# Kernel optimization log

Measured on AMD Instinct MI355X. Metric: run time of the kernel, lower is better.

## Reference

```python
import jax, jax.numpy as jnp
import numpy as np

T, H, E, I, K = 2048, 2048, 16, 512, 2
ROUTED_SCALE = 1.5   # config.moe_router_scaling_factor
SWIGLU_LIMIT = 7.0   # config.swiglu_limits[layer_id]


def setup_inputs() -> dict:
    key = jax.random.key(0)
    k1, k2, k3, k4, k5 = jax.random.split(key, 5)
    hidden_states = jax.random.normal(k1, (T, H), jnp.float32)
    gate_w = jax.random.normal(k2, (E, H), jnp.float32) * 0.02
    router_bias = jax.random.normal(k3, (E,), jnp.float32) * 0.01
    w13 = jax.random.normal(k4, (E, 2 * I, H), jnp.float32) * 0.02  # [gate; up] fused
    w2 = jax.random.normal(k5, (E, H, I), jnp.float32) * 0.02
    return {"hidden_states": hidden_states, "gate_w": gate_w,
            "router_bias": router_bias, "w13": w13, "w2": w2, "top_k": K}


def reference(hidden_states, gate_w, router_bias, w13, w2, top_k):
    n_tok = hidden_states.shape[0]
    n_exp = gate_w.shape[0]
    # fp32 gate (need_fp32_gate=True)
    router_logits = hidden_states.astype(jnp.float32) @ gate_w.T          # [T, E]
    scores = jax.nn.sigmoid(router_logits)
    # correction bias only affects expert choice, not the combine weights
    _, topk_ids = jax.lax.top_k(scores + router_bias[None, :], top_k)     # [T, K]
    topk_w = jnp.take_along_axis(scores, topk_ids, axis=1)                # [T, K]
    topk_w = topk_w / jnp.sum(topk_w, axis=1, keepdims=True)              # renormalize
    topk_w = topk_w * ROUTED_SCALE
    # scatter routing weights into dense per-expert combine weights [T, E]
    comb = jnp.zeros((n_tok, n_exp), jnp.float32)
    comb = comb.at[jnp.arange(n_tok)[:, None], topk_ids].add(topk_w)
    # expert SwiGLU MLPs, dense over experts (zero combine weight == not routed)
    gu = jnp.einsum('th,eoh->teo', hidden_states, w13)                    # [T, E, 2I]
    g, u = jnp.split(gu, 2, axis=-1)
    g = jnp.minimum(g, SWIGLU_LIMIT)                                      # gemm1_clamp_limit
    u = jnp.clip(u, -SWIGLU_LIMIT, SWIGLU_LIMIT)
    act = g * jax.nn.sigmoid(g) * u                                       # silu(gate) * up
    expert_out = jnp.einsum('tei,ehi->teh', act, w2)                      # [T, E, H]
    return jnp.einsum('teh,te->th', expert_out, comb)                     # [T, H]
```

## Files before the change

kernel.cpp:

```cpp
#include <hip/hip_runtime.h>
#include <hip/hip_bf16.h>
#include <math.h>

#define T_TOK 2048
#define H_DIM 2048
#define E_EXP 16
#define I_DIM 512
#define TWO_I 1024
#define ROUTED_SCALE 1.5f
#define SWIGLU_LIMIT 7.0f

#define BM 128
#define KC 32
#define MAX_TILES 48
#define SLOTS 6144

typedef __attribute__((ext_vector_type(8))) short bf16x8;
typedef __attribute__((ext_vector_type(4))) float f32x4;
typedef unsigned short u16;

__device__ inline u16 f2bf(float f) {
    return __builtin_bit_cast(u16, __float2bfloat16(f));
}
__device__ inline ushort4 pack4(float4 a) {
    ushort4 v;
    v.x = f2bf(a.x); v.y = f2bf(a.y); v.z = f2bf(a.z); v.w = f2bf(a.w);
    return v;
}
__device__ inline bf16x8 cvt8(float4 a, float4 b) {
    bf16x8 v;
    v[0] = (short)f2bf(a.x); v[1] = (short)f2bf(a.y);
    v[2] = (short)f2bf(a.z); v[3] = (short)f2bf(a.w);
    v[4] = (short)f2bf(b.x); v[5] = (short)f2bf(b.y);
    v[6] = (short)f2bf(b.z); v[7] = (short)f2bf(b.w);
    return v;
}

__device__ inline void gload16(const u16* g, u16* l) {
    __builtin_amdgcn_global_load_lds(
        (const __attribute__((address_space(1))) void*)(g),
        (__attribute__((address_space(3))) void*)(l), 16, 0, 0);
}
#define SCHED0() __builtin_amdgcn_sched_barrier(0)

__global__ __launch_bounds__(256) void router_kernel(
    const float* __restrict__ hs, const float* __restrict__ gw,
    const float* __restrict__ bias, int* cnt, int* tok_list, float* w_list,
    u16* __restrict__ hs_bf)
{
    int wave = threadIdx.x >> 6;
    int lane = threadIdx.x & 63;
    int t = blockIdx.x * 4 + wave;
    if (t >= T_TOK) return;
    const float* x = hs + (size_t)t * H_DIM;

    float acc[E_EXP];
#pragma unroll
    for (int e = 0; e < E_EXP; ++e) acc[e] = 0.f;

#pragma unroll 2
    for (int c = 0; c < 8; ++c) {
        int col = c * 256 + lane * 4;
        float4 xv = *(const float4*)(x + col);
        *(ushort4*)(hs_bf + (size_t)t * H_DIM + col) = pack4(xv);
#pragma unroll
        for (int e = 0; e < E_EXP; ++e) {
            float4 gv = *(const float4*)(gw + (size_t)e * H_DIM + col);
            acc[e] = fmaf(xv.x, gv.x, acc[e]);
            acc[e] = fmaf(xv.y, gv.y, acc[e]);
            acc[e] = fmaf(xv.z, gv.z, acc[e]);
            acc[e] = fmaf(xv.w, gv.w, acc[e]);
        }
    }
#pragma unroll
    for (int e = 0; e < E_EXP; ++e) {
        for (int m = 32; m >= 1; m >>= 1)
            acc[e] += __shfl_xor(acc[e], m, 64);
    }
    if (lane == 0) {
        float sc[E_EXP], bsc[E_EXP];
#pragma unroll
        for (int e = 0; e < E_EXP; ++e) {
            sc[e] = 1.f / (1.f + expf(-acc[e]));
            bsc[e] = sc[e] + bias[e];
        }
        int e0 = 0; float b0 = bsc[0];
#pragma unroll
        for (int e = 1; e < E_EXP; ++e) if (bsc[e] > b0) { b0 = bsc[e]; e0 = e; }
        int e1 = -1; float b1 = -1e30f;
#pragma unroll
        for (int e = 0; e < E_EXP; ++e) {
            if (e == e0) continue;
            if (bsc[e] > b1) { b1 = bsc[e]; e1 = e; }
        }
        float s0 = sc[e0], s1 = sc[e1];
        float inv = ROUTED_SCALE / (s0 + s1);
        int p0 = atomicAdd(&cnt[e0], 1);
        tok_list[e0 * T_TOK + p0] = t;
        w_list[e0 * T_TOK + p0] = s0 * inv;
        int p1 = atomicAdd(&cnt[e1], 1);
        tok_list[e1 * T_TOK + p1] = t;
        w_list[e1 * T_TOK + p1] = s1 * inv;
    }
}

__global__ void scatter_build(const int* __restrict__ cnt,
    const int* __restrict__ tok_list, const float* __restrict__ w_list,
    int* A_tok, float* A_w, int* tile_e, int* tile_r0)
{
    int c[E_EXP], offs[E_EXP + 1];
    offs[0] = 0;
#pragma unroll
    for (int e = 0; e < E_EXP; ++e) {
        c[e] = cnt[e];
        offs[e + 1] = offs[e] + ((c[e] + BM - 1) & ~(BM - 1));
    }
    int idx = blockIdx.x * 256 + threadIdx.x;
    int e = idx >> 11;
    int pos = idx & (T_TOK - 1);
    int ce = c[e];
    int pe = (ce + BM - 1) & ~(BM - 1);
    if (pos < ce) {
        A_tok[offs[e] + pos] = tok_list[idx];
        A_w[offs[e] + pos] = w_list[idx];
    } else if (pos < pe) {
        A_tok[offs[e] + pos] = -1;
        A_w[offs[e] + pos] = 0.f;
    }
    if (idx == 0) {
        int nt = 0;
        for (int ee = 0; ee < E_EXP; ++ee) {
            int ntile = (c[ee] + BM - 1) >> 7;
            for (int j = 0; j < ntile; ++j) {
                tile_e[nt] = ee;
                tile_r0[nt] = offs[ee] + j * BM;
                ++nt;
            }
        }
        for (; nt < MAX_TILES; ++nt) tile_e[nt] = -1;
    }
}

__global__ __launch_bounds__(256, 3) void gemm1_gu(
    const u16* __restrict__ hs_bf, const float* __restrict__ w13,
    const int* __restrict__ A_tok, const int* __restrict__ tile_e,
    const int* __restrict__ tile_r0, float* __restrict__ gu_part)
{
    int b = blockIdx.x;
    int y = b & 7;
    int kspl = (b >> 3) & 1;
    int tile = b >> 4;
    int e = tile_e[tile];
    if (e < 0) return;
    int row0 = tile_r0[tile];
    int i0 = y * 64;
    int k0base = kspl * (H_DIM / 2);
    int tid = threadIdx.x;

    __shared__ u16 Xs[2][4096];
    __shared__ u16 Gs[2][2048];
    __shared__ u16 Us[2][2048];

    const int l = tid & 63, w = tid >> 6;

    const u16* sX[2]; int dX[2];
#pragma unroll
    for (int j = 0; j < 2; ++j) {
        int row = w * 32 + j * 16 + (l >> 2);
        int tk = A_tok[row0 + row]; if (tk < 0) tk = 0;
        int sg = (l & 3) ^ ((l >> 3) & 3);
        sX[j] = hs_bf + (size_t)tk * H_DIM + k0base + sg * 8;
        dX[j] = (w * 32 + j * 16) * 32;
    }
#define X_STAGE(bb, t) do { int ko = (t) * KC; \
    gload16(sX[0] + ko, &Xs[bb][dX[0]]); gload16(sX[1] + ko, &Xs[bb][dX[1]]); } while (0)

    const int wr = tid >> 2;
    const int wg = tid & 3;
    const int wsk = (wg ^ ((wr >> 1) & 3)) * 8;
    const float* gsrc = w13 + ((size_t)e * TWO_I + i0 + wr) * H_DIM + k0base + wsk;
    const float* usrc = gsrc + (size_t)I_DIM * H_DIM;
    const int wdst = wr * 32 + wg * 8;

    float4 gA, gB, uA, uB;
#define W_LOAD(t) do { int ko = (t) * KC; \
    gA = *(const float4*)(gsrc + ko); gB = *(const float4*)(gsrc + ko + 4); \
    uA = *(const float4*)(usrc + ko); uB = *(const float4*)(usrc + ko + 4); } while (0)
#define W_WRITE(bb) do { \
    *(bf16x8*)&Gs[bb][wdst] = cvt8(gA, gB); \
    *(bf16x8*)&Us[bb][wdst] = cvt8(uA, uB); } while (0)

    const int wm = w >> 1, wn = w & 1;
    const int lr = l & 15, lg = l >> 4;
    const int swz = (lg ^ ((lr >> 1) & 3)) * 8;
    int ix[4], ib[2];
#pragma unroll
    for (int m = 0; m < 4; ++m) ix[m] = (wm * 64 + m * 16 + lr) * 32 + swz;
#pragma unroll
    for (int n = 0; n < 2; ++n) ib[n] = (wn * 32 + n * 16 + lr) * 32 + swz;

    const f32x4 Z4 = {0.f, 0.f, 0.f, 0.f};
    f32x4 aG[4][2], aU[4][2];
#pragma unroll
    for (int m = 0; m < 4; ++m)
#pragma unroll
        for (int n = 0; n < 2; ++n) { aG[m][n] = Z4; aU[m][n] = Z4; }

    W_LOAD(0);
    X_STAGE(0, 0);
    W_WRITE(0);
    __syncthreads();
    int cur = 0;
    const int NT = (H_DIM / 2) / KC;
    for (int t = 0; t < NT; ++t) {
        const bool more = (t + 1 < NT);
        if (more) {
            X_STAGE(cur ^ 1, t + 1);
            W_LOAD(t + 1);
            SCHED0();
        }
        {
            bf16x8 a0 = *(const bf16x8*)&Xs[cur][ix[0]];
            bf16x8 a1 = *(const bf16x8*)&Xs[cur][ix[1]];
            bf16x8 a2 = *(const bf16x8*)&Xs[cur][ix[2]];
            bf16x8 a3 = *(const bf16x8*)&Xs[cur][ix[3]];
            bf16x8 g0 = *(const bf16x8*)&Gs[cur][ib[0]];
            bf16x8 g1 = *(const bf16x8*)&Gs[cur][ib[1]];
            bf16x8 u0 = *(const bf16x8*)&Us[cur][ib[0]];
            bf16x8 u1 = *(const bf16x8*)&Us[cur][ib[1]];
            aG[0][0] = __builtin_amdgcn_mfma_f32_16x16x32_bf16(a0, g0, aG[0][0], 0, 0, 0);
            aG[0][1] = __builtin_amdgcn_mfma_f32_16x16x32_bf16(a0, g1, aG[0][1], 0, 0, 0);
            aG[1][0] = __builtin_amdgcn_mfma_f32_16x16x32_bf16(a1, g0, aG[1][0], 0, 0, 0);
            aG[1][1] = __builtin_amdgcn_mfma_f32_16x16x32_bf16(a1, g1, aG[1][1], 0, 0, 0);
            aG[2][0] = __builtin_amdgcn_mfma_f32_16x16x32_bf16(a2, g0, aG[2][0], 0, 0, 0);
            aG[2][1] = __builtin_amdgcn_mfma_f32_16x16x32_bf16(a2, g1, aG[2][1], 0, 0, 0);
            aG[3][0] = __builtin_amdgcn_mfma_f32_16x16x32_bf16(a3, g0, aG[3][0], 0, 0, 0);
            aG[3][1] = __builtin_amdgcn_mfma_f32_16x16x32_bf16(a3, g1, aG[3][1], 0, 0, 0);
            aU[0][0] = __builtin_amdgcn_mfma_f32_16x16x32_bf16(a0, u0, aU[0][0], 0, 0, 0);
            aU[0][1] = __builtin_amdgcn_mfma_f32_16x16x32_bf16(a0, u1, aU[0][1], 0, 0, 0);
            aU[1][0] = __builtin_amdgcn_mfma_f32_16x16x32_bf16(a1, u0, aU[1][0], 0, 0, 0);
            aU[1][1] = __builtin_amdgcn_mfma_f32_16x16x32_bf16(a1, u1, aU[1][1], 0, 0, 0);
            aU[2][0] = __builtin_amdgcn_mfma_f32_16x16x32_bf16(a2, u0, aU[2][0], 0, 0, 0);
            aU[2][1] = __builtin_amdgcn_mfma_f32_16x16x32_bf16(a2, u1, aU[2][1], 0, 0, 0);
            aU[3][0] = __builtin_amdgcn_mfma_f32_16x16x32_bf16(a3, u0, aU[3][0], 0, 0, 0);
            aU[3][1] = __builtin_amdgcn_mfma_f32_16x16x32_bf16(a3, u1, aU[3][1], 0, 0, 0);
        }
        if (more) W_WRITE(cur ^ 1);
        __syncthreads();
        cur ^= 1;
    }
#undef X_STAGE
#undef W_LOAD
#undef W_WRITE

    float* gp = gu_part + (size_t)kspl * SLOTS * TWO_I;
#pragma unroll
    for (int m = 0; m < 4; ++m)
#pragma unroll
        for (int n = 0; n < 2; ++n) {
            int col = i0 + wn * 32 + n * 16 + lr;
            int sbase = row0 + wm * 64 + m * 16 + lg * 4;
#pragma unroll
            for (int q = 0; q < 4; ++q) {
                gp[(size_t)(sbase + q) * TWO_I + col]         = aG[m][n][q];
                gp[(size_t)(sbase + q) * TWO_I + I_DIM + col] = aU[m][n][q];
            }
        }
}

__global__ __launch_bounds__(256) void swiglu_pass(
    const float* __restrict__ gu_part, u16* __restrict__ act)
{
    int idx = blockIdx.x * 256 + threadIdx.x;
    int slot = idx >> 7;
    int i4 = (idx & 127) << 2;
    const float* p0 = gu_part + (size_t)slot * TWO_I + i4;
    const float* p1 = p0 + (size_t)SLOTS * TWO_I;
    float4 g0 = *(const float4*)p0;
    float4 g1 = *(const float4*)p1;
    float4 u0 = *(const float4*)(p0 + I_DIM);
    float4 u1 = *(const float4*)(p1 + I_DIM);
    float4 r;
    {
        float g = fminf(g0.x + g1.x, SWIGLU_LIMIT);
        float u = fminf(fmaxf(u0.x + u1.x, -SWIGLU_LIMIT), SWIGLU_LIMIT);
        r.x = g * (1.f / (1.f + __expf(-g))) * u;
    }
    {
        float g = fminf(g0.y + g1.y, SWIGLU_LIMIT);
        float u = fminf(fmaxf(u0.y + u1.y, -SWIGLU_LIMIT), SWIGLU_LIMIT);
        r.y = g * (1.f / (1.f + __expf(-g))) * u;
    }
    {
        float g = fminf(g0.z + g1.z, SWIGLU_LIMIT);
        float u = fminf(fmaxf(u0.z + u1.z, -SWIGLU_LIMIT), SWIGLU_LIMIT);
        r.z = g * (1.f / (1.f + __expf(-g))) * u;
    }
    {
        float g = fminf(g0.w + g1.w, SWIGLU_LIMIT);
        float u = fminf(fmaxf(u0.w + u1.w, -SWIGLU_LIMIT), SWIGLU_LIMIT);
        r.w = g * (1.f / (1.f + __expf(-g))) * u;
    }
    *(ushort4*)(act + (size_t)slot * I_DIM + i4) = pack4(r);
}

__global__ __launch_bounds__(256, 3) void gemm2_scatter(
    const u16* __restrict__ act, const float* __restrict__ w2,
    const int* __restrict__ A_tok, const float* __restrict__ A_w,
    const int* __restrict__ tile_e, const int* __restrict__ tile_r0,
    float* __restrict__ out)
{
    int b = blockIdx.x;
    int y = (b & 7) * 2 + ((b >> 3) & 1);
    int tile = b >> 4;
    int e = tile_e[tile];
    if (e < 0) return;
    int row0 = tile_r0[tile];
    int h0 = y * 128;
    int tid = threadIdx.x;

    __shared__ u16 As[2][4096];
    __shared__ u16 Bs[2][4096];

    const int l = tid & 63, w = tid >> 6;

    const u16* sA[2]; int dA[2];
#pragma unroll
    for (int j = 0; j < 2; ++j) {
        int row = w * 32 + j * 16 + (l >> 2);
        int sg = (l & 3) ^ ((l >> 3) & 3);
        sA[j] = act + (size_t)(row0 + row) * I_DIM + sg * 8;
        dA[j] = (w * 32 + j * 16) * 32;
    }
#define A_STAGE(bb, t) do { int ko = (t) * KC; \
    gload16(sA[0] + ko, &As[bb][dA[0]]); gload16(sA[1] + ko, &As[bb][dA[1]]); } while (0)

    const int wr = tid >> 1;
    const int wg0 = (tid & 1) * 2;
    const float* bsrc = w2 + ((size_t)e * H_DIM + h0 + wr) * I_DIM;
    const int sk0 = ((wg0)     ^ ((wr >> 1) & 3)) * 8;
    const int sk1 = ((wg0 + 1) ^ ((wr >> 1) & 3)) * 8;
    const int wd0 = wr * 32 + wg0 * 8;

    float4 b0a, b0b, b1a, b1b;
#define B_LOAD(t) do { int ko = (t) * KC; \
    b0a = *(const float4*)(bsrc + ko + sk0); b0b = *(const float4*)(bsrc + ko + sk0 + 4); \
    b1a = *(const float4*)(bsrc + ko + sk1); b1b = *(const float4*)(bsrc + ko + sk1 + 4); } while (0)
#define B_WRITE(bb) do { \
    *(bf16x8*)&Bs[bb][wd0]     = cvt8(b0a, b0b); \
    *(bf16x8*)&Bs[bb][wd0 + 8] = cvt8(b1a, b1b); } while (0)

    const int wm = w >> 1, wn = w & 1;
    const int lr = l & 15, lg = l >> 4;
    const int swz = (lg ^ ((lr >> 1) & 3)) * 8;
    int ix[4], ib[4];
#pragma unroll
    for (int m = 0; m < 4; ++m) ix[m] = (wm * 64 + m * 16 + lr) * 32 + swz;
#pragma unroll
    for (int n = 0; n < 4; ++n) ib[n] = (wn * 64 + n * 16 + lr) * 32 + swz;

    const f32x4 Z4 = {0.f, 0.f, 0.f, 0.f};
    f32x4 acc[4][4];
#pragma unroll
    for (int m = 0; m < 4; ++m)
#pragma unroll
        for (int n = 0; n < 4; ++n) acc[m][n] = Z4;

    B_LOAD(0);
    A_STAGE(0, 0);
    B_WRITE(0);
    __syncthreads();
    int cur = 0;
    const int NT = I_DIM / KC;
    for (int t = 0; t < NT; ++t) {
        const bool more = (t + 1 < NT);
        if (more) {
            A_STAGE(cur ^ 1, t + 1);
            B_LOAD(t + 1);
            SCHED0();
        }
        {
            bf16x8 a[4], bb[4];
#pragma unroll
            for (int m = 0; m < 4; ++m) a[m] = *(const bf16x8*)&As[cur][ix[m]];
#pragma unroll
            for (int n = 0; n < 4; ++n) bb[n] = *(const bf16x8*)&Bs[cur][ib[n]];
#pragma unroll
            for (int m = 0; m < 4; ++m)
#pragma unroll
                for (int n = 0; n < 4; ++n)
                    acc[m][n] = __builtin_amdgcn_mfma_f32_16x16x32_bf16(a[m], bb[n], acc[m][n], 0, 0, 0);
        }
        if (more) B_WRITE(cur ^ 1);
        __syncthreads();
        cur ^= 1;
    }
#undef A_STAGE
#undef B_LOAD
#undef B_WRITE

#pragma unroll
    for (int m = 0; m < 4; ++m)
#pragma unroll
        for (int n = 0; n < 4; ++n) {
            int col = h0 + wn * 64 + n * 16 + lr;
            int sbase = row0 + wm * 64 + m * 16 + lg * 4;
#pragma unroll
            for (int q = 0; q < 4; ++q) {
                int slot = sbase + q;
                int tok = A_tok[slot];
                if (tok >= 0)
                    atomicAdd(&out[(size_t)tok * H_DIM + col], acc[m][n][q] * A_w[slot]);
            }
        }
}

extern "C" void kernel_launch(void* const* d_in, const int* in_sizes, int n_in,
                              void* d_out, int out_size, void* d_ws, size_t ws_size,
                              hipStream_t stream) {
    const float* hs   = (const float*)d_in[0];
    const float* gw   = (const float*)d_in[1];
    const float* bias = (const float*)d_in[2];
    const float* w13  = (const float*)d_in[3];
    const float* w2   = (const float*)d_in[4];
    float* out = (float*)d_out;

    char* ws = (char*)d_ws;
    int*   cnt      = (int*)(ws + 0);
    int*   tile_e   = (int*)(ws + 64);
    int*   tile_r0  = (int*)(ws + 320);
    int*   tok_list = (int*)(ws + 1024);
    float* w_list   = (float*)(ws + 132096);
    int*   A_tok    = (int*)(ws + 263168);
    float* A_w      = (float*)(ws + 287744);
    u16*   act      = (u16*)(ws + 315392);
    u16*   hs_bf    = (u16*)(ws + 6606848);
    float* gu_part  = (float*)(ws + 14995456);

    hipMemsetAsync(d_out, 0, (size_t)T_TOK * H_DIM * sizeof(float), stream);
    hipMemsetAsync(cnt, 0, 64, stream);

    router_kernel<<<T_TOK / 4, 256, 0, stream>>>(hs, gw, bias, cnt, tok_list, w_list, hs_bf);
    scatter_build<<<(E_EXP * T_TOK) / 256, 256, 0, stream>>>(cnt, tok_list, w_list, A_tok, A_w, tile_e, tile_r0);

    gemm1_gu<<<MAX_TILES * 8 * 2, 256, 0, stream>>>(hs_bf, w13, A_tok, tile_e, tile_r0, gu_part);
    swiglu_pass<<<SLOTS * I_DIM / 4 / 256, 256, 0, stream>>>(gu_part, act);
    gemm2_scatter<<<MAX_TILES * 16, 256, 0, stream>>>(act, w2, A_tok, A_w, tile_e, tile_r0, out);
}
```

Measured before the change: 209.3 us.

## Retile gemm2 to 128x64 with KC=64, split router rows, skip unused swiglu slots

The router now splits each token's hidden dimension across two waves and combines the partial sums in shared memory, which doubles the number of blocks. The swiglu pass exits early for padded slots beyond the real slot count, which scatter_build now writes out. gemm2 is retiled: the N tile shrinks to 64 with a K chunk of 64 and an XOR-swizzled LDS layout, twice as many blocks are launched, and blocks are ordered so tiles are interleaved across groups. This aims for more parallelism and less wasted work, at the cost of re-reading the activation tiles more often and fewer MFMAs per LDS load.

```diff
diff --git a/kernel.cpp b/kernel.cpp
--- a/kernel.cpp
+++ b/kernel.cpp
@@ -12,6 +12,7 @@
 
 #define BM 128
 #define KC 32
+#define KC2 64
 #define MAX_TILES 48
 #define SLOTS 6144
 
@@ -43,29 +44,33 @@
 }
 #define SCHED0() __builtin_amdgcn_sched_barrier(0)
 
+#define SWZ(row, k) ((row) * 64 + ((k) ^ (((row) & 7) << 3)))
+
 __global__ __launch_bounds__(256) void router_kernel(
     const float* __restrict__ hs, const float* __restrict__ gw,
     const float* __restrict__ bias, int* cnt, int* tok_list, float* w_list,
     u16* __restrict__ hs_bf)
 {
-    int wave = threadIdx.x >> 6;
+    int w = threadIdx.x >> 6;
     int lane = threadIdx.x & 63;
-    int t = blockIdx.x * 4 + wave;
-    if (t >= T_TOK) return;
-    const float* x = hs + (size_t)t * H_DIM;
+    int t = blockIdx.x * 2 + (w >> 1);
+    int kh = w & 1;
+    const float* x = hs + (size_t)t * H_DIM + kh * 1024;
+    const float* gwb = gw + kh * 1024;
+    u16* hb = hs_bf + (size_t)t * H_DIM + kh * 1024;
 
     float acc[E_EXP];
 #pragma unroll
     for (int e = 0; e < E_EXP; ++e) acc[e] = 0.f;
 
-#pragma unroll 2
-    for (int c = 0; c < 8; ++c) {
+#pragma unroll
+    for (int c = 0; c < 4; ++c) {
         int col = c * 256 + lane * 4;
         float4 xv = *(const float4*)(x + col);
-        *(ushort4*)(hs_bf + (size_t)t * H_DIM + col) = pack4(xv);
+        *(ushort4*)(hb + col) = pack4(xv);
 #pragma unroll
         for (int e = 0; e < E_EXP; ++e) {
-            float4 gv = *(const float4*)(gw + (size_t)e * H_DIM + col);
+            float4 gv = *(const float4*)(gwb + (size_t)e * H_DIM + col);
             acc[e] = fmaf(xv.x, gv.x, acc[e]);
             acc[e] = fmaf(xv.y, gv.y, acc[e]);
             acc[e] = fmaf(xv.z, gv.z, acc[e]);
@@ -77,11 +82,18 @@
         for (int m = 32; m >= 1; m >>= 1)
             acc[e] += __shfl_xor(acc[e], m, 64);
     }
+    __shared__ float part[4][E_EXP];
     if (lane == 0) {
+#pragma unroll
+        for (int e = 0; e < E_EXP; ++e) part[w][e] = acc[e];
+    }
+    __syncthreads();
+    if (kh == 0 && lane == 0) {
         float sc[E_EXP], bsc[E_EXP];
 #pragma unroll
         for (int e = 0; e < E_EXP; ++e) {
-            sc[e] = 1.f / (1.f + expf(-acc[e]));
+            float s = part[w][e] + part[w + 1][e];
+            sc[e] = 1.f / (1.f + expf(-s));
             bsc[e] = sc[e] + bias[e];
         }
         int e0 = 0; float b0 = bsc[0];
@@ -106,7 +118,7 @@
 
 __global__ void scatter_build(const int* __restrict__ cnt,
     const int* __restrict__ tok_list, const float* __restrict__ w_list,
-    int* A_tok, float* A_w, int* tile_e, int* tile_r0)
+    int* A_tok, float* A_w, int* tile_e, int* tile_r0, int* n_slots)
 {
     int c[E_EXP], offs[E_EXP + 1];
     offs[0] = 0;
@@ -138,6 +150,7 @@
             }
         }
         for (; nt < MAX_TILES; ++nt) tile_e[nt] = -1;
+        *n_slots = offs[E_EXP];
     }
 }
 
@@ -269,10 +282,12 @@
 }
 
 __global__ __launch_bounds__(256) void swiglu_pass(
-    const float* __restrict__ gu_part, u16* __restrict__ act)
+    const float* __restrict__ gu_part, const int* __restrict__ n_slots,
+    u16* __restrict__ act)
 {
     int idx = blockIdx.x * 256 + threadIdx.x;
     int slot = idx >> 7;
+    if (slot >= *n_slots) return;
     int i4 = (idx & 127) << 2;
     const float* p0 = gu_part + (size_t)slot * TWO_I + i4;
     const float* p1 = p0 + (size_t)SLOTS * TWO_I;
@@ -311,67 +326,81 @@
     float* __restrict__ out)
 {
     int b = blockIdx.x;
-    int y = (b & 7) * 2 + ((b >> 3) & 1);
-    int tile = b >> 4;
+    int id = (b & 7) * 192 + (b >> 3);
+    int tile = id % MAX_TILES;
+    int y = id / MAX_TILES;
     int e = tile_e[tile];
     if (e < 0) return;
     int row0 = tile_r0[tile];
-    int h0 = y * 128;
+    int h0 = y * 64;
     int tid = threadIdx.x;
 
-    __shared__ u16 As[2][4096];
+    __shared__ u16 As[2][8192];
     __shared__ u16 Bs[2][4096];
 
     const int l = tid & 63, w = tid >> 6;
 
-    const u16* sA[2]; int dA[2];
-#pragma unroll
-    for (int j = 0; j < 2; ++j) {
-        int row = w * 32 + j * 16 + (l >> 2);
-        int sg = (l & 3) ^ ((l >> 3) & 3);
-        sA[j] = act + (size_t)(row0 + row) * I_DIM + sg * 8;
-        dA[j] = (w * 32 + j * 16) * 32;
-    }
-#define A_STAGE(bb, t) do { int ko = (t) * KC; \
-    gload16(sA[0] + ko, &As[bb][dA[0]]); gload16(sA[1] + ko, &As[bb][dA[1]]); } while (0)
-
-    const int wr = tid >> 1;
-    const int wg0 = (tid & 1) * 2;
-    const float* bsrc = w2 + ((size_t)e * H_DIM + h0 + wr) * I_DIM;
-    const int sk0 = ((wg0)     ^ ((wr >> 1) & 3)) * 8;
-    const int sk1 = ((wg0 + 1) ^ ((wr >> 1) & 3)) * 8;
-    const int wd0 = wr * 32 + wg0 * 8;
-
-    float4 b0a, b0b, b1a, b1b;
-#define B_LOAD(t) do { int ko = (t) * KC; \
-    b0a = *(const float4*)(bsrc + ko + sk0); b0b = *(const float4*)(bsrc + ko + sk0 + 4); \
-    b1a = *(const float4*)(bsrc + ko + sk1); b1b = *(const float4*)(bsrc + ko + sk1 + 4); } while (0)
+    const int rlo = l >> 3;
+    const int c8 = (l & 7) << 3;
+    const int ksrc = c8 ^ (rlo << 3);
+    const u16* sA[4];
+#pragma unroll
+    for (int j = 0; j < 4; ++j) {
+        int row = w * 32 + j * 8 + rlo;
+        sA[j] = act + (size_t)(row0 + row) * I_DIM + ksrc;
+    }
+    const int dA = w * 2048;
+
+#define A_STAGE(bb, t) do { int ko = (t) * KC2; \
+    gload16(sA[0] + ko, &As[bb][dA]); \
+    gload16(sA[1] + ko, &As[bb][dA + 512]); \
+    gload16(sA[2] + ko, &As[bb][dA + 1024]); \
+    gload16(sA[3] + ko, &As[bb][dA + 1536]); } while (0)
+
+    const int srow = tid >> 4;
+    const int sc4  = tid & 15;
+    const int kphys = (sc4 * 4) ^ ((srow & 7) << 3);
+    const int sbase = srow * 64 + kphys;
+    const float* bsrc = w2 + ((size_t)e * H_DIM + h0 + srow) * I_DIM + sc4 * 4;
+
+    float4 bld[4];
+#define B_LOAD(t) do { int k0 = (t) * KC2; \
+    bld[0] = *(const float4*)(bsrc + k0); \
+    bld[1] = *(const float4*)(bsrc + k0 + 16 * I_DIM); \
+    bld[2] = *(const float4*)(bsrc + k0 + 32 * I_DIM); \
+    bld[3] = *(const float4*)(bsrc + k0 + 48 * I_DIM); } while (0)
+
 #define B_WRITE(bb) do { \
-    *(bf16x8*)&Bs[bb][wd0]     = cvt8(b0a, b0b); \
-    *(bf16x8*)&Bs[bb][wd0 + 8] = cvt8(b1a, b1b); } while (0)
+    *(ushort4*)&Bs[bb][sbase]        = pack4(bld[0]); \
+    *(ushort4*)&Bs[bb][sbase + 1024] = pack4(bld[1]); \
+    *(ushort4*)&Bs[bb][sbase + 2048] = pack4(bld[2]); \
+    *(ushort4*)&Bs[bb][sbase + 3072] = pack4(bld[3]); } while (0)
 
     const int wm = w >> 1, wn = w & 1;
     const int lr = l & 15, lg = l >> 4;
-    const int swz = (lg ^ ((lr >> 1) & 3)) * 8;
-    int ix[4], ib[4];
-#pragma unroll
-    for (int m = 0; m < 4; ++m) ix[m] = (wm * 64 + m * 16 + lr) * 32 + swz;
-#pragma unroll
-    for (int n = 0; n < 4; ++n) ib[n] = (wn * 64 + n * 16 + lr) * 32 + swz;
+    int ia[4][2], ib2[2][2];
+#pragma unroll
+    for (int kh = 0; kh < 2; ++kh) {
+        int e2 = kh * 32 + lg * 8;
+#pragma unroll
+        for (int m = 0; m < 4; ++m) ia[m][kh] = SWZ(wm * 64 + m * 16 + lr, e2);
+#pragma unroll
+        for (int n = 0; n < 2; ++n) ib2[n][kh] = SWZ(wn * 32 + n * 16 + lr, e2);
+    }
 
     const f32x4 Z4 = {0.f, 0.f, 0.f, 0.f};
-    f32x4 acc[4][4];
+    f32x4 acc[4][2];
 #pragma unroll
     for (int m = 0; m < 4; ++m)
 #pragma unroll
-        for (int n = 0; n < 4; ++n) acc[m][n] = Z4;
+        for (int n = 0; n < 2; ++n) acc[m][n] = Z4;
 
     B_LOAD(0);
     A_STAGE(0, 0);
     B_WRITE(0);
     __syncthreads();
     int cur = 0;
-    const int NT = I_DIM / KC;
+    const int NT = I_DIM / KC2;
     for (int t = 0; t < NT; ++t) {
         const bool more = (t + 1 < NT);
         if (more) {
@@ -379,17 +408,22 @@
             B_LOAD(t + 1);
             SCHED0();
         }
-        {
-            bf16x8 a[4], bb[4];
-#pragma unroll
-            for (int m = 0; m < 4; ++m) a[m] = *(const bf16x8*)&As[cur][ix[m]];
-#pragma unroll
-            for (int n = 0; n < 4; ++n) bb[n] = *(const bf16x8*)&Bs[cur][ib[n]];
-#pragma unroll
-            for (int m = 0; m < 4; ++m)
-#pragma unroll
-                for (int n = 0; n < 4; ++n)
-                    acc[m][n] = __builtin_amdgcn_mfma_f32_16x16x32_bf16(a[m], bb[n], acc[m][n], 0, 0, 0);
+#pragma unroll
+        for (int kh = 0; kh < 2; ++kh) {
+            bf16x8 a0 = *(const bf16x8*)&As[cur][ia[0][kh]];
+            bf16x8 a1 = *(const bf16x8*)&As[cur][ia[1][kh]];
+            bf16x8 a2 = *(const bf16x8*)&As[cur][ia[2][kh]];
+            bf16x8 a3 = *(const bf16x8*)&As[cur][ia[3][kh]];
+            bf16x8 b0 = *(const bf16x8*)&Bs[cur][ib2[0][kh]];
+            bf16x8 b1 = *(const bf16x8*)&Bs[cur][ib2[1][kh]];
+            acc[0][0] = __builtin_amdgcn_mfma_f32_16x16x32_bf16(a0, b0, acc[0][0], 0, 0, 0);
+            acc[0][1] = __builtin_amdgcn_mfma_f32_16x16x32_bf16(a0, b1, acc[0][1], 0, 0, 0);
+            acc[1][0] = __builtin_amdgcn_mfma_f32_16x16x32_bf16(a1, b0, acc[1][0], 0, 0, 0);
+            acc[1][1] = __builtin_amdgcn_mfma_f32_16x16x32_bf16(a1, b1, acc[1][1], 0, 0, 0);
+            acc[2][0] = __builtin_amdgcn_mfma_f32_16x16x32_bf16(a2, b0, acc[2][0], 0, 0, 0);
+            acc[2][1] = __builtin_amdgcn_mfma_f32_16x16x32_bf16(a2, b1, acc[2][1], 0, 0, 0);
+            acc[3][0] = __builtin_amdgcn_mfma_f32_16x16x32_bf16(a3, b0, acc[3][0], 0, 0, 0);
+            acc[3][1] = __builtin_amdgcn_mfma_f32_16x16x32_bf16(a3, b1, acc[3][1], 0, 0, 0);
         }
         if (more) B_WRITE(cur ^ 1);
         __syncthreads();
@@ -402,12 +436,12 @@
 #pragma unroll
     for (int m = 0; m < 4; ++m)
 #pragma unroll
-        for (int n = 0; n < 4; ++n) {
-            int col = h0 + wn * 64 + n * 16 + lr;
-            int sbase = row0 + wm * 64 + m * 16 + lg * 4;
+        for (int n = 0; n < 2; ++n) {
+            int col = h0 + wn * 32 + n * 16 + lr;
+            int sb = row0 + wm * 64 + m * 16 + lg * 4;
 #pragma unroll
             for (int q = 0; q < 4; ++q) {
-                int slot = sbase + q;
+                int slot = sb + q;
                 int tok = A_tok[slot];
                 if (tok >= 0)
                     atomicAdd(&out[(size_t)tok * H_DIM + col], acc[m][n][q] * A_w[slot]);
@@ -427,8 +461,9 @@
 
     char* ws = (char*)d_ws;
     int*   cnt      = (int*)(ws + 0);
-    int*   tile_e   = (int*)(ws + 64);
-    int*   tile_r0  = (int*)(ws + 320);
+    int*   n_slots  = (int*)(ws + 64);
+    int*   tile_e   = (int*)(ws + 128);
+    int*   tile_r0  = (int*)(ws + 384);
     int*   tok_list = (int*)(ws + 1024);
     float* w_list   = (float*)(ws + 132096);
     int*   A_tok    = (int*)(ws + 263168);
@@ -440,10 +475,10 @@
     hipMemsetAsync(d_out, 0, (size_t)T_TOK * H_DIM * sizeof(float), stream);
     hipMemsetAsync(cnt, 0, 64, stream);
 
-    router_kernel<<<T_TOK / 4, 256, 0, stream>>>(hs, gw, bias, cnt, tok_list, w_list, hs_bf);
-    scatter_build<<<(E_EXP * T_TOK) / 256, 256, 0, stream>>>(cnt, tok_list, w_list, A_tok, A_w, tile_e, tile_r0);
+    router_kernel<<<T_TOK / 2, 256, 0, stream>>>(hs, gw, bias, cnt, tok_list, w_list, hs_bf);
+    scatter_build<<<(E_EXP * T_TOK) / 256, 256, 0, stream>>>(cnt, tok_list, w_list, A_tok, A_w, tile_e, tile_r0, n_slots);
 
     gemm1_gu<<<MAX_TILES * 8 * 2, 256, 0, stream>>>(hs_bf, w13, A_tok, tile_e, tile_r0, gu_part);
-    swiglu_pass<<<SLOTS * I_DIM / 4 / 256, 256, 0, stream>>>(gu_part, act);
-    gemm2_scatter<<<MAX_TILES * 16, 256, 0, stream>>>(act, w2, A_tok, A_w, tile_e, tile_r0, out);
-}
+    swiglu_pass<<<SLOTS * I_DIM / 4 / 256, 256, 0, stream>>>(gu_part, n_slots, act);
+    gemm2_scatter<<<MAX_TILES * 32, 256, 0, stream>>>(act, w2, A_tok, A_w, tile_e, tile_r0, out);
+}
```

Measured after the change: 205.0 us. -2.0%, faster.
